# Optimization experiments

Hardware: AMD Instinct MI355X
Metric: run time of the kernel (lower is better)

The kernel has to match this reference:

```python
import jax, jax.numpy as jnp
import numpy as np

# Sizes (see shape_source): N samples, D=Config.dim, H=D//2, E question types, C classes/type
N, D, H, E, C = 65536, 768, 384, 8, 8


def setup_inputs() -> dict:
    key = jax.random.key(0)
    k_x, k_t, k_w1, k_w2 = jax.random.split(key, 4)
    x = jax.random.normal(k_x, (N, D), dtype=jnp.float32)
    question_types = jax.random.randint(k_t, (N,), 0, E, dtype=jnp.int32)
    # Stacked per-type MLP head parameters (E experts)
    W1 = jax.random.normal(k_w1, (E, D, H), dtype=jnp.float32) * 0.02
    b1 = jnp.zeros((E, H), dtype=jnp.float32)
    W2 = jax.random.normal(k_w2, (E, H, C), dtype=jnp.float32) * 0.02
    b2 = jnp.zeros((E, C), dtype=jnp.float32)
    return {"x": x, "W1": W1, "b1": b1, "W2": W2, "b2": b2,
            "question_types": question_types}


def reference(x, W1, b1, W2, b2, question_types):
    # Per-sample routed 2-layer MLP head: logits_i = MLP_{type_i}(x_i).
    # Dropout is eval-mode identity. Dense-per-expert compute + mask select
    # (standard MoE reference; E is a small fixed loop, not a data-dim loop).
    n_experts = W1.shape[0]
    out = jnp.zeros((x.shape[0], W2.shape[-1]), dtype=x.dtype)
    for e in range(n_experts):
        h = jax.nn.relu(x @ W1[e] + b1[e])        # [N, H]
        logits = h @ W2[e] + b2[e]                # [N, C]
        out = jnp.where((question_types == e)[:, None], logits, out)
    return out
```

## Files before the change

### kernel.cpp

```cpp
#include <hip/hip_runtime.h>

typedef short s16x8 __attribute__((ext_vector_type(8)));
typedef float f32x4 __attribute__((ext_vector_type(4)));

#define N_SAMPLES 65536
#define DIM 768
#define HID 384
#define NEXP 8
#define NCLS 8

#define WS_CNT    0
#define WS_BUCKET 1024
#define WS_W1T    (WS_BUCKET + NEXP * N_SAMPLES * 4)
#define WS_W2T    (WS_W1T + NEXP * HID * DIM * 2)

__device__ __forceinline__ unsigned short f2bf(float f) {
  union { float f; unsigned u; } v; v.f = f;
  unsigned r = v.u + 0x7fffu + ((v.u >> 16) & 1u);
  return (unsigned short)(r >> 16);
}

__global__ void k_transpose_w1(const float* __restrict__ W1,
                               unsigned short* __restrict__ W1T) {
  __shared__ float tile[32][33];
  const int e = blockIdx.z, k0 = blockIdx.x * 32, j0 = blockIdx.y * 32;
  const int tx = threadIdx.x, ty = threadIdx.y;
  const float* src = W1 + (size_t)e * DIM * HID;
#pragma unroll
  for (int i = 0; i < 32; i += 8)
    tile[ty + i][tx] = src[(size_t)(k0 + ty + i) * HID + j0 + tx];
  __syncthreads();
  unsigned short* dst = W1T + (size_t)e * HID * DIM;
#pragma unroll
  for (int i = 0; i < 32; i += 8)
    dst[(size_t)(j0 + ty + i) * DIM + k0 + tx] = f2bf(tile[tx][ty + i]);
}

__global__ void k_w2_cnt(const float* __restrict__ W2,
                         unsigned short* __restrict__ W2T,
                         int* __restrict__ cnt) {
  const int e = blockIdx.x, j = threadIdx.x;
  if (e == 0 && j < NEXP) cnt[j] = 0;
#pragma unroll
  for (int c = 0; c < NCLS; ++c)
    W2T[((size_t)e * NCLS + c) * HID + j] = f2bf(W2[((size_t)e * HID + j) * NCLS + c]);
}

__global__ void k_scatter_init(const int* __restrict__ qt, const float* __restrict__ b2,
                               int* __restrict__ cnt, int* __restrict__ bucket,
                               float* __restrict__ out) {
  __shared__ int lcnt[NEXP], lbase[NEXP];
  const int t = threadIdx.x;
  const int i = blockIdx.x * 256 + t;
  if (t < NEXP) lcnt[t] = 0;
  __syncthreads();
  const int e = qt[i];
  const int rank = atomicAdd(&lcnt[e], 1);
  __syncthreads();
  if (t < NEXP) lbase[t] = atomicAdd(&cnt[t], lcnt[t]);
  __syncthreads();
  bucket[(size_t)e * N_SAMPLES + lbase[e] + rank] = i;
  const float4* b2v = (const float4*)(b2 + e * NCLS);
  float4* ov = (float4*)(out + (size_t)i * NCLS);
  ov[0] = b2v[0];
  ov[1] = b2v[1];
}

#define GLL16(g, l)                                                        \
  __builtin_amdgcn_global_load_lds(                                        \
      (__attribute__((address_space(1))) void*)(void*)(g),                 \
      (__attribute__((address_space(3))) void*)(l), 16, 0, 0)

__global__ __launch_bounds__(256, 2) void k_moe_gemm(
    const float* __restrict__ x, const unsigned short* __restrict__ W1T,
    const float* __restrict__ b1, const unsigned short* __restrict__ W2T,
    const int* __restrict__ cnt, const int* __restrict__ bucket,
    float* __restrict__ out) {
  __shared__ __align__(16) short smem[17408];
  __shared__ __align__(16) short W2s[16 * 128];
  __shared__ float b1s[128];
  __shared__ int idxs[128];
  short* As = smem;
  short* Bs = smem + 4096;
  short* Hs = smem;

  const int e = blockIdx.z;
  const int n_e = cnt[e];
  const int j0 = blockIdx.x * 128;
  const int t = threadIdx.x;
  const int lane = t & 63;
  const int wave = t >> 6;
  const int lrow = lane & 15;
  const int quad = lane >> 4;
  const int lk = quad * 8;
  const int mbase = (wave & 1) * 64;
  const int nbase = (wave >> 1) * 64;

  {
    const int c = t >> 4, jj = (t & 15) * 8;
    s16x8 wv = {0, 0, 0, 0, 0, 0, 0, 0};
    if (c < NCLS) wv = *(const s16x8*)&W2T[((size_t)e * NCLS + c) * HID + j0 + jj];
    *(s16x8*)&W2s[c * 128 + jj] = wv;
  }
  if (t < 128) b1s[t] = b1[e * HID + j0 + t];

  for (int rt = blockIdx.y; rt * 128 < n_e; rt += gridDim.y) {
    const int row0 = rt * 128;
    __syncthreads();
    if (t < 128) {
      const int slot = row0 + t;
      idxs[t] = bucket[(size_t)e * N_SAMPLES + ((slot < n_e) ? slot : row0)];
    }
    __syncthreads();

    const float* xrow = x + (size_t)idxs[t >> 1] * DIM + (t & 1) * 16;
    const unsigned short* g0 = W1T + ((size_t)(e * HID + j0 + (t >> 2)) * DIM + (t & 3) * 8);
    const unsigned short* g1 = W1T + ((size_t)(e * HID + j0 + 64 + (t >> 2)) * DIM + (t & 3) * 8);

    f32x4 acc[4][4];
#pragma unroll
    for (int mi = 0; mi < 4; ++mi)
#pragma unroll
      for (int ni = 0; ni < 4; ++ni) acc[mi][ni] = (f32x4){0.f, 0.f, 0.f, 0.f};

    float4 v0 = ((const float4*)xrow)[0];
    float4 v1 = ((const float4*)xrow)[1];
    float4 v2 = ((const float4*)xrow)[2];
    float4 v3 = ((const float4*)xrow)[3];

    for (int ks = 0; ks < 24; ++ks) {
      s16x8 p0 = {(short)f2bf(v0.x), (short)f2bf(v0.y), (short)f2bf(v0.z), (short)f2bf(v0.w),
                  (short)f2bf(v1.x), (short)f2bf(v1.y), (short)f2bf(v1.z), (short)f2bf(v1.w)};
      s16x8 p1 = {(short)f2bf(v2.x), (short)f2bf(v2.y), (short)f2bf(v2.z), (short)f2bf(v2.w),
                  (short)f2bf(v3.x), (short)f2bf(v3.y), (short)f2bf(v3.z), (short)f2bf(v3.w)};
      *(s16x8*)&As[t * 16] = p0;
      *(s16x8*)&As[t * 16 + 8] = p1;
      GLL16(g0 + ks * 32, &Bs[t * 8]);
      GLL16(g1 + ks * 32, &Bs[2048 + t * 8]);
      __syncthreads();
      if (ks < 23) {
        const float4* nx = (const float4*)(xrow + (ks + 1) * 32);
        v0 = nx[0]; v1 = nx[1]; v2 = nx[2]; v3 = nx[3];
      }
      s16x8 bfr[4];
#pragma unroll
      for (int ni = 0; ni < 4; ++ni)
        bfr[ni] = *(const s16x8*)&Bs[(nbase + ni * 16 + lrow) * 32 + lk];
#pragma unroll
      for (int mi = 0; mi < 4; ++mi) {
        s16x8 afr = *(const s16x8*)&As[(mbase + mi * 16 + lrow) * 32 + lk];
#pragma unroll
        for (int ni = 0; ni < 4; ++ni)
          acc[mi][ni] = __builtin_amdgcn_mfma_f32_16x16x32_bf16(afr, bfr[ni], acc[mi][ni], 0, 0, 0);
      }
      __syncthreads();
    }

#pragma unroll
    for (int ni = 0; ni < 4; ++ni) {
      const int jl = nbase + ni * 16 + lrow;
      const float bias = b1s[jl];
#pragma unroll
      for (int mi = 0; mi < 4; ++mi) {
        const int mrow = mbase + mi * 16 + quad * 4;
#pragma unroll
        for (int r = 0; r < 4; ++r) {
          float v = acc[mi][ni][r] + bias;
          v = v > 0.f ? v : 0.f;
          Hs[(mrow + r) * 136 + jl] = (short)f2bf(v);
        }
      }
    }
    __syncthreads();

#pragma unroll
    for (int p = 0; p < 2; ++p) {
      const int mt = wave * 2 + p;
      f32x4 acc2 = (f32x4){0.f, 0.f, 0.f, 0.f};
#pragma unroll
      for (int kk = 0; kk < 4; ++kk) {
        s16x8 af = *(const s16x8*)&Hs[(mt * 16 + lrow) * 136 + kk * 32 + lk];
        s16x8 bf = *(const s16x8*)&W2s[lrow * 128 + kk * 32 + lk];
        acc2 = __builtin_amdgcn_mfma_f32_16x16x32_bf16(af, bf, acc2, 0, 0, 0);
      }
      if (lrow < NCLS) {
#pragma unroll
        for (int r = 0; r < 4; ++r) {
          const int m = mt * 16 + quad * 4 + r;
          if (row0 + m < n_e)
            atomicAdd(out + (size_t)idxs[m] * NCLS + lrow, acc2[r]);
        }
      }
    }
  }
}

extern "C" void kernel_launch(void* const* d_in, const int* in_sizes, int n_in,
                              void* d_out, int out_size, void* d_ws, size_t ws_size,
                              hipStream_t stream) {
  const float* x  = (const float*)d_in[0];
  const float* W1 = (const float*)d_in[1];
  const float* b1 = (const float*)d_in[2];
  const float* W2 = (const float*)d_in[3];
  const float* b2 = (const float*)d_in[4];
  const int* qt   = (const int*)d_in[5];
  float* out = (float*)d_out;
  char* ws = (char*)d_ws;

  int* cnt = (int*)(ws + WS_CNT);
  int* bucket = (int*)(ws + WS_BUCKET);
  unsigned short* W1T = (unsigned short*)(ws + WS_W1T);
  unsigned short* W2T = (unsigned short*)(ws + WS_W2T);

  k_transpose_w1<<<dim3(24, 12, 8), dim3(32, 8), 0, stream>>>(W1, W1T);
  k_w2_cnt<<<dim3(8), dim3(384), 0, stream>>>(W2, W2T, cnt);
  k_scatter_init<<<dim3(256), dim3(256), 0, stream>>>(qt, b2, cnt, bucket, out);
  k_moe_gemm<<<dim3(3, 96, 8), dim3(256), 0, stream>>>(x, W1T, b1, W2T, cnt, bucket, out);
}
```

Measured before the change: 377.9 us.

## Double-buffer GEMM LDS tiles, merge setup kernels, retune grid and occupancy

The main GEMM loop now keeps two LDS buffers for the A and B tiles. Each step issues the next W1 tile's global-to-LDS load and x prefetch, then runs the MFMAs on the current buffer, which leaves one barrier per k-step instead of two. The W2 transpose and counter zeroing move into the existing scatter and W1-transpose kernels, removing one launch. Launch bounds go from 2 to 3 blocks per CU and grid.y drops from 96 to 32, so each block loops over more row tiles. The tradeoffs are more LDS-resident state and higher register pressure at the raised occupancy target.

```diff
diff --git a/kernel.cpp b/kernel.cpp
--- a/kernel.cpp
+++ b/kernel.cpp
@@ -21,7 +21,11 @@
 }
 
 __global__ void k_transpose_w1(const float* __restrict__ W1,
-                               unsigned short* __restrict__ W1T) {
+                               unsigned short* __restrict__ W1T,
+                               int* __restrict__ cnt) {
+  if (blockIdx.x == 0 && blockIdx.y == 0 && blockIdx.z == 0 &&
+      threadIdx.y == 0 && threadIdx.x < NEXP)
+    cnt[threadIdx.x] = 0;
   __shared__ float tile[32][33];
   const int e = blockIdx.z, k0 = blockIdx.x * 32, j0 = blockIdx.y * 32;
   const int tx = threadIdx.x, ty = threadIdx.y;
@@ -36,21 +40,21 @@
     dst[(size_t)(j0 + ty + i) * DIM + k0 + tx] = f2bf(tile[tx][ty + i]);
 }
 
-__global__ void k_w2_cnt(const float* __restrict__ W2,
-                         unsigned short* __restrict__ W2T,
-                         int* __restrict__ cnt) {
-  const int e = blockIdx.x, j = threadIdx.x;
-  if (e == 0 && j < NEXP) cnt[j] = 0;
-#pragma unroll
-  for (int c = 0; c < NCLS; ++c)
-    W2T[((size_t)e * NCLS + c) * HID + j] = f2bf(W2[((size_t)e * HID + j) * NCLS + c]);
-}
-
 __global__ void k_scatter_init(const int* __restrict__ qt, const float* __restrict__ b2,
+                               const float* __restrict__ W2,
                                int* __restrict__ cnt, int* __restrict__ bucket,
-                               float* __restrict__ out) {
+                               float* __restrict__ out, unsigned short* __restrict__ W2T) {
+  const int t = threadIdx.x;
+  if (blockIdx.x >= 256) {
+    const int e = blockIdx.x - 256;
+    for (int j = t; j < HID; j += 256)
+#pragma unroll
+      for (int c = 0; c < NCLS; ++c)
+        W2T[((size_t)e * NCLS + c) * HID + j] =
+            f2bf(W2[((size_t)e * HID + j) * NCLS + c]);
+    return;
+  }
   __shared__ int lcnt[NEXP], lbase[NEXP];
-  const int t = threadIdx.x;
   const int i = blockIdx.x * 256 + t;
   if (t < NEXP) lcnt[t] = 0;
   __syncthreads();
@@ -71,7 +75,38 @@
       (__attribute__((address_space(1))) void*)(void*)(g),                 \
       (__attribute__((address_space(3))) void*)(l), 16, 0, 0)
 
-__global__ __launch_bounds__(256, 2) void k_moe_gemm(
+#define K_STEP(KS, AC, BC, BN)                                                  \
+  {                                                                             \
+    s16x8 p0 = {(short)f2bf(v0.x), (short)f2bf(v0.y), (short)f2bf(v0.z),        \
+                (short)f2bf(v0.w), (short)f2bf(v1.x), (short)f2bf(v1.y),        \
+                (short)f2bf(v1.z), (short)f2bf(v1.w)};                          \
+    s16x8 p1 = {(short)f2bf(v2.x), (short)f2bf(v2.y), (short)f2bf(v2.z),        \
+                (short)f2bf(v2.w), (short)f2bf(v3.x), (short)f2bf(v3.y),        \
+                (short)f2bf(v3.z), (short)f2bf(v3.w)};                          \
+    *(s16x8*)&(AC)[t * 16] = p0;                                                \
+    *(s16x8*)&(AC)[t * 16 + 8] = p1;                                            \
+    __syncthreads();                                                            \
+    if ((KS) + 1 < 24) {                                                        \
+      GLL16(g0 + ((KS) + 1) * 32, &(BN)[t * 8]);                                \
+      GLL16(g1 + ((KS) + 1) * 32, &(BN)[2048 + t * 8]);                         \
+      const float4* nx = (const float4*)(xrow + ((KS) + 1) * 32);               \
+      v0 = nx[0]; v1 = nx[1]; v2 = nx[2]; v3 = nx[3];                           \
+    }                                                                           \
+    s16x8 bfr[4];                                                               \
+    _Pragma("unroll")                                                           \
+    for (int ni = 0; ni < 4; ++ni)                                              \
+      bfr[ni] = *(const s16x8*)&(BC)[(nbase + ni * 16 + lrow) * 32 + lk];       \
+    _Pragma("unroll")                                                           \
+    for (int mi = 0; mi < 4; ++mi) {                                            \
+      s16x8 afr = *(const s16x8*)&(AC)[(mbase + mi * 16 + lrow) * 32 + lk];     \
+      _Pragma("unroll")                                                         \
+      for (int ni = 0; ni < 4; ++ni)                                            \
+        acc[mi][ni] = __builtin_amdgcn_mfma_f32_16x16x32_bf16(                  \
+            afr, bfr[ni], acc[mi][ni], 0, 0, 0);                                \
+    }                                                                           \
+  }
+
+__global__ __launch_bounds__(256, 3) void k_moe_gemm(
     const float* __restrict__ x, const unsigned short* __restrict__ W1T,
     const float* __restrict__ b1, const unsigned short* __restrict__ W2T,
     const int* __restrict__ cnt, const int* __restrict__ bucket,
@@ -80,8 +115,10 @@
   __shared__ __align__(16) short W2s[16 * 128];
   __shared__ float b1s[128];
   __shared__ int idxs[128];
-  short* As = smem;
-  short* Bs = smem + 4096;
+  short* As0 = smem;
+  short* As1 = smem + 4096;
+  short* Bs0 = smem + 8192;
+  short* Bs1 = smem + 12288;
   short* Hs = smem;
 
   const int e = blockIdx.z;
@@ -127,34 +164,15 @@
     float4 v1 = ((const float4*)xrow)[1];
     float4 v2 = ((const float4*)xrow)[2];
     float4 v3 = ((const float4*)xrow)[3];
-
-    for (int ks = 0; ks < 24; ++ks) {
-      s16x8 p0 = {(short)f2bf(v0.x), (short)f2bf(v0.y), (short)f2bf(v0.z), (short)f2bf(v0.w),
-                  (short)f2bf(v1.x), (short)f2bf(v1.y), (short)f2bf(v1.z), (short)f2bf(v1.w)};
-      s16x8 p1 = {(short)f2bf(v2.x), (short)f2bf(v2.y), (short)f2bf(v2.z), (short)f2bf(v2.w),
-                  (short)f2bf(v3.x), (short)f2bf(v3.y), (short)f2bf(v3.z), (short)f2bf(v3.w)};
-      *(s16x8*)&As[t * 16] = p0;
-      *(s16x8*)&As[t * 16 + 8] = p1;
-      GLL16(g0 + ks * 32, &Bs[t * 8]);
-      GLL16(g1 + ks * 32, &Bs[2048 + t * 8]);
-      __syncthreads();
-      if (ks < 23) {
-        const float4* nx = (const float4*)(xrow + (ks + 1) * 32);
-        v0 = nx[0]; v1 = nx[1]; v2 = nx[2]; v3 = nx[3];
-      }
-      s16x8 bfr[4];
-#pragma unroll
-      for (int ni = 0; ni < 4; ++ni)
-        bfr[ni] = *(const s16x8*)&Bs[(nbase + ni * 16 + lrow) * 32 + lk];
-#pragma unroll
-      for (int mi = 0; mi < 4; ++mi) {
-        s16x8 afr = *(const s16x8*)&As[(mbase + mi * 16 + lrow) * 32 + lk];
-#pragma unroll
-        for (int ni = 0; ni < 4; ++ni)
-          acc[mi][ni] = __builtin_amdgcn_mfma_f32_16x16x32_bf16(afr, bfr[ni], acc[mi][ni], 0, 0, 0);
-      }
-      __syncthreads();
-    }
+    GLL16(g0, &Bs0[t * 8]);
+    GLL16(g1, &Bs0[2048 + t * 8]);
+
+    for (int ks = 0; ks < 24; ks += 2) {
+      K_STEP(ks, As0, Bs0, Bs1)
+      K_STEP(ks + 1, As1, Bs1, Bs0)
+    }
+
+    __syncthreads();
 
 #pragma unroll
     for (int ni = 0; ni < 4; ++ni) {
@@ -212,8 +230,7 @@
   unsigned short* W1T = (unsigned short*)(ws + WS_W1T);
   unsigned short* W2T = (unsigned short*)(ws + WS_W2T);
 
-  k_transpose_w1<<<dim3(24, 12, 8), dim3(32, 8), 0, stream>>>(W1, W1T);
-  k_w2_cnt<<<dim3(8), dim3(384), 0, stream>>>(W2, W2T, cnt);
-  k_scatter_init<<<dim3(256), dim3(256), 0, stream>>>(qt, b2, cnt, bucket, out);
-  k_moe_gemm<<<dim3(3, 96, 8), dim3(256), 0, stream>>>(x, W1T, b1, W2T, cnt, bucket, out);
-}
+  k_transpose_w1<<<dim3(24, 12, 8), dim3(32, 8), 0, stream>>>(W1, W1T, cnt);
+  k_scatter_init<<<dim3(264), dim3(256), 0, stream>>>(qt, b2, W2, cnt, bucket, out, W2T);
+  k_moe_gemm<<<dim3(3, 32, 8), dim3(256), 0, stream>>>(x, W1T, b1, W2T, cnt, bucket, out);
+}
```

After: 382.7 us. About the same (+1.3%).

## Compute full hidden width per block to avoid x reloads and atomics

Applied to the files above, without the earlier changes.

Each block now covers all 384 hidden units for a 64-row tile of one expert, not a 128-column slice. Each x row is therefore read and converted to bf16 once instead of three times, and the second layer writes logits directly with the b2 bias instead of using atomicAdd onto a bias-initialised output. It adds LDS double buffering for the A and B tiles, a faster round-to-nearest bf16 packing via perm, and folds the W2 conversion and counter reset into other kernels, removing one launch. Per-block LDS use grows, and the bf16 rounding of activations changes slightly.

```diff
diff --git a/kernel.cpp b/kernel.cpp
--- a/kernel.cpp
+++ b/kernel.cpp
@@ -12,7 +12,6 @@
 #define WS_CNT    0
 #define WS_BUCKET 1024
 #define WS_W1T    (WS_BUCKET + NEXP * N_SAMPLES * 4)
-#define WS_W2T    (WS_W1T + NEXP * HID * DIM * 2)
 
 __device__ __forceinline__ unsigned short f2bf(float f) {
   union { float f; unsigned u; } v; v.f = f;
@@ -20,8 +19,23 @@
   return (unsigned short)(r >> 16);
 }
 
+__device__ __forceinline__ short f2bf_fast(float f) {
+  union { float f; unsigned u; } v; v.f = f;
+  return (short)((v.u + 0x8000u) >> 16);
+}
+
+__device__ __forceinline__ unsigned cvt2(float a, float b) {
+  union { float f; unsigned u; } ua, ub;
+  ua.f = a; ub.f = b;
+  return __builtin_amdgcn_perm(ub.u + 0x8000u, ua.u + 0x8000u, 0x07060302u);
+}
+
 __global__ void k_transpose_w1(const float* __restrict__ W1,
-                               unsigned short* __restrict__ W1T) {
+                               unsigned short* __restrict__ W1T,
+                               int* __restrict__ cnt) {
+  if (blockIdx.x == 0 && blockIdx.y == 0 && blockIdx.z == 0 &&
+      threadIdx.y == 0 && threadIdx.x < NEXP)
+    cnt[threadIdx.x] = 0;
   __shared__ float tile[32][33];
   const int e = blockIdx.z, k0 = blockIdx.x * 32, j0 = blockIdx.y * 32;
   const int tx = threadIdx.x, ty = threadIdx.y;
@@ -36,19 +50,8 @@
     dst[(size_t)(j0 + ty + i) * DIM + k0 + tx] = f2bf(tile[tx][ty + i]);
 }
 
-__global__ void k_w2_cnt(const float* __restrict__ W2,
-                         unsigned short* __restrict__ W2T,
-                         int* __restrict__ cnt) {
-  const int e = blockIdx.x, j = threadIdx.x;
-  if (e == 0 && j < NEXP) cnt[j] = 0;
-#pragma unroll
-  for (int c = 0; c < NCLS; ++c)
-    W2T[((size_t)e * NCLS + c) * HID + j] = f2bf(W2[((size_t)e * HID + j) * NCLS + c]);
-}
-
-__global__ void k_scatter_init(const int* __restrict__ qt, const float* __restrict__ b2,
-                               int* __restrict__ cnt, int* __restrict__ bucket,
-                               float* __restrict__ out) {
+__global__ void k_scatter(const int* __restrict__ qt, int* __restrict__ cnt,
+                          int* __restrict__ bucket) {
   __shared__ int lcnt[NEXP], lbase[NEXP];
   const int t = threadIdx.x;
   const int i = blockIdx.x * 256 + t;
@@ -60,10 +63,6 @@
   if (t < NEXP) lbase[t] = atomicAdd(&cnt[t], lcnt[t]);
   __syncthreads();
   bucket[(size_t)e * N_SAMPLES + lbase[e] + rank] = i;
-  const float4* b2v = (const float4*)(b2 + e * NCLS);
-  float4* ov = (float4*)(out + (size_t)i * NCLS);
-  ov[0] = b2v[0];
-  ov[1] = b2v[1];
 }
 
 #define GLL16(g, l)                                                        \
@@ -71,127 +70,143 @@
       (__attribute__((address_space(1))) void*)(void*)(g),                 \
       (__attribute__((address_space(3))) void*)(l), 16, 0, 0)
 
+#define GLLB(KS, BUF)                                                      \
+  _Pragma("unroll") for (int rep = 0; rep < 6; ++rep)                      \
+      GLL16(bp + (size_t)rep * 64 * DIM + (KS) * 32, &(BUF)[(rep * 256 + t) * 8]);
+
+#define ASTORE(BUF, LO, HI)                                                \
+  {                                                                        \
+    unsigned p01 = cvt2((LO).x, (LO).y), p23 = cvt2((LO).z, (LO).w);       \
+    unsigned p45 = cvt2((HI).x, (HI).y), p67 = cvt2((HI).z, (HI).w);       \
+    uint4 pk = {p01, p23, p45, p67};                                       \
+    *(uint4*)&(BUF)[ar * 40 + aq * 8] = pk;                                \
+  }
+
+#define COMPUTE(AS, BS)                                                    \
+  {                                                                        \
+    s16x8 bfr[6];                                                          \
+    _Pragma("unroll") for (int ni = 0; ni < 6; ++ni)                       \
+        bfr[ni] = *(const s16x8*)&(BS)[(wave * 96 + ni * 16 + lrow) * 32 + quad * 8]; \
+    _Pragma("unroll") for (int mi = 0; mi < 4; ++mi) {                     \
+      s16x8 afr = *(const s16x8*)&(AS)[(mi * 16 + lrow) * 40 + quad * 8];  \
+      _Pragma("unroll") for (int ni = 0; ni < 6; ++ni)                     \
+          acc[mi][ni] = __builtin_amdgcn_mfma_f32_16x16x32_bf16(           \
+              afr, bfr[ni], acc[mi][ni], 0, 0, 0);                         \
+    }                                                                      \
+  }
+
 __global__ __launch_bounds__(256, 2) void k_moe_gemm(
     const float* __restrict__ x, const unsigned short* __restrict__ W1T,
-    const float* __restrict__ b1, const unsigned short* __restrict__ W2T,
-    const int* __restrict__ cnt, const int* __restrict__ bucket,
-    float* __restrict__ out) {
-  __shared__ __align__(16) short smem[17408];
-  __shared__ __align__(16) short W2s[16 * 128];
-  __shared__ float b1s[128];
-  __shared__ int idxs[128];
-  short* As = smem;
-  short* Bs = smem + 4096;
-  short* Hs = smem;
-
-  const int e = blockIdx.z;
+    const float* __restrict__ b1, const float* __restrict__ W2,
+    const float* __restrict__ b2, const int* __restrict__ cnt,
+    const int* __restrict__ bucket, float* __restrict__ out) {
+  __shared__ __align__(16) short smem[29696];
+  __shared__ __align__(16) short W2s[16 * 392];
+  __shared__ float b1s[HID];
+  __shared__ float b2s[NCLS];
+  short* As0 = smem;
+  short* As1 = smem + 2560;
+  short* Bs0 = smem + 5120;
+  short* Bs1 = smem + 17408;
+  short* Hs  = smem;
+
+  const int e = blockIdx.x;
   const int n_e = cnt[e];
-  const int j0 = blockIdx.x * 128;
   const int t = threadIdx.x;
   const int lane = t & 63;
   const int wave = t >> 6;
   const int lrow = lane & 15;
   const int quad = lane >> 4;
-  const int lk = quad * 8;
-  const int mbase = (wave & 1) * 64;
-  const int nbase = (wave >> 1) * 64;
-
-  {
-    const int c = t >> 4, jj = (t & 15) * 8;
-    s16x8 wv = {0, 0, 0, 0, 0, 0, 0, 0};
-    if (c < NCLS) wv = *(const s16x8*)&W2T[((size_t)e * NCLS + c) * HID + j0 + jj];
-    *(s16x8*)&W2s[c * 128 + jj] = wv;
-  }
-  if (t < 128) b1s[t] = b1[e * HID + j0 + t];
-
-  for (int rt = blockIdx.y; rt * 128 < n_e; rt += gridDim.y) {
-    const int row0 = rt * 128;
+  const int ar = t >> 2;
+  const int aq = t & 3;
+
+  for (int j = t; j < HID; j += 256) {
+    b1s[j] = b1[e * HID + j];
+    const float* wr = W2 + ((size_t)e * HID + j) * NCLS;
+#pragma unroll
+    for (int c = 0; c < NCLS; ++c) W2s[c * 392 + j] = (short)f2bf(wr[c]);
+#pragma unroll
+    for (int c = NCLS; c < 16; ++c) W2s[c * 392 + j] = 0;
+  }
+  if (t < NCLS) b2s[t] = b2[e * NCLS + t];
+
+  const unsigned short* bp = W1T + ((size_t)e * HID + (t >> 2)) * DIM + (t & 3) * 8;
+
+  for (int rt = blockIdx.y; rt * 64 < n_e; rt += gridDim.y) {
+    const int row0 = rt * 64;
+    int slot = row0 + ar;
+    if (slot >= n_e) slot = n_e - 1;
+    const int aidx = bucket[(size_t)e * N_SAMPLES + slot];
+    const float* ap = x + (size_t)aidx * DIM + aq * 8;
+
+    f32x4 acc[4][6];
+#pragma unroll
+    for (int mi = 0; mi < 4; ++mi)
+#pragma unroll
+      for (int ni = 0; ni < 6; ++ni) acc[mi][ni] = (f32x4){0.f, 0.f, 0.f, 0.f};
+
+    float4 a0lo = ((const float4*)ap)[0];
+    float4 a0hi = ((const float4*)(ap + 4))[0];
+    GLLB(0, Bs0)
+    ASTORE(As0, a0lo, a0hi)
+    float4 a1lo = ((const float4*)(ap + 32))[0];
+    float4 a1hi = ((const float4*)(ap + 36))[0];
+
+    for (int ks = 0; ks < 24; ks += 2) {
+      __syncthreads();
+      if (ks + 1 < 24) { GLLB(ks + 1, Bs1) ASTORE(As1, a1lo, a1hi) }
+      if (ks + 2 < 24) {
+        a0lo = ((const float4*)(ap + (ks + 2) * 32))[0];
+        a0hi = ((const float4*)(ap + (ks + 2) * 32 + 4))[0];
+      }
+      COMPUTE(As0, Bs0)
+      __syncthreads();
+      if (ks + 2 < 24) { GLLB(ks + 2, Bs0) ASTORE(As0, a0lo, a0hi) }
+      if (ks + 3 < 24) {
+        a1lo = ((const float4*)(ap + (ks + 3) * 32))[0];
+        a1hi = ((const float4*)(ap + (ks + 3) * 32 + 4))[0];
+      }
+      COMPUTE(As1, Bs1)
+    }
+
     __syncthreads();
-    if (t < 128) {
-      const int slot = row0 + t;
-      idxs[t] = bucket[(size_t)e * N_SAMPLES + ((slot < n_e) ? slot : row0)];
-    }
-    __syncthreads();
-
-    const float* xrow = x + (size_t)idxs[t >> 1] * DIM + (t & 1) * 16;
-    const unsigned short* g0 = W1T + ((size_t)(e * HID + j0 + (t >> 2)) * DIM + (t & 3) * 8);
-    const unsigned short* g1 = W1T + ((size_t)(e * HID + j0 + 64 + (t >> 2)) * DIM + (t & 3) * 8);
-
-    f32x4 acc[4][4];
+
 #pragma unroll
     for (int mi = 0; mi < 4; ++mi)
 #pragma unroll
-      for (int ni = 0; ni < 4; ++ni) acc[mi][ni] = (f32x4){0.f, 0.f, 0.f, 0.f};
-
-    float4 v0 = ((const float4*)xrow)[0];
-    float4 v1 = ((const float4*)xrow)[1];
-    float4 v2 = ((const float4*)xrow)[2];
-    float4 v3 = ((const float4*)xrow)[3];
-
-    for (int ks = 0; ks < 24; ++ks) {
-      s16x8 p0 = {(short)f2bf(v0.x), (short)f2bf(v0.y), (short)f2bf(v0.z), (short)f2bf(v0.w),
-                  (short)f2bf(v1.x), (short)f2bf(v1.y), (short)f2bf(v1.z), (short)f2bf(v1.w)};
-      s16x8 p1 = {(short)f2bf(v2.x), (short)f2bf(v2.y), (short)f2bf(v2.z), (short)f2bf(v2.w),
-                  (short)f2bf(v3.x), (short)f2bf(v3.y), (short)f2bf(v3.z), (short)f2bf(v3.w)};
-      *(s16x8*)&As[t * 16] = p0;
-      *(s16x8*)&As[t * 16 + 8] = p1;
-      GLL16(g0 + ks * 32, &Bs[t * 8]);
-      GLL16(g1 + ks * 32, &Bs[2048 + t * 8]);
-      __syncthreads();
-      if (ks < 23) {
-        const float4* nx = (const float4*)(xrow + (ks + 1) * 32);
-        v0 = nx[0]; v1 = nx[1]; v2 = nx[2]; v3 = nx[3];
-      }
-      s16x8 bfr[4];
-#pragma unroll
-      for (int ni = 0; ni < 4; ++ni)
-        bfr[ni] = *(const s16x8*)&Bs[(nbase + ni * 16 + lrow) * 32 + lk];
-#pragma unroll
-      for (int mi = 0; mi < 4; ++mi) {
-        s16x8 afr = *(const s16x8*)&As[(mbase + mi * 16 + lrow) * 32 + lk];
-#pragma unroll
-        for (int ni = 0; ni < 4; ++ni)
-          acc[mi][ni] = __builtin_amdgcn_mfma_f32_16x16x32_bf16(afr, bfr[ni], acc[mi][ni], 0, 0, 0);
-      }
-      __syncthreads();
-    }
-
-#pragma unroll
-    for (int ni = 0; ni < 4; ++ni) {
-      const int jl = nbase + ni * 16 + lrow;
-      const float bias = b1s[jl];
-#pragma unroll
-      for (int mi = 0; mi < 4; ++mi) {
-        const int mrow = mbase + mi * 16 + quad * 4;
+      for (int ni = 0; ni < 6; ++ni) {
+        const int j = wave * 96 + ni * 16 + lrow;
+        const float bias = b1s[j];
 #pragma unroll
         for (int r = 0; r < 4; ++r) {
           float v = acc[mi][ni][r] + bias;
           v = v > 0.f ? v : 0.f;
-          Hs[(mrow + r) * 136 + jl] = (short)f2bf(v);
+          Hs[(mi * 16 + quad * 4 + r) * 392 + j] = f2bf_fast(v);
+        }
+      }
+    __syncthreads();
+
+    {
+      f32x4 acc2 = (f32x4){0.f, 0.f, 0.f, 0.f};
+#pragma unroll
+      for (int kk = 0; kk < 12; ++kk) {
+        s16x8 af = *(const s16x8*)&Hs[(wave * 16 + lrow) * 392 + kk * 32 + quad * 8];
+        s16x8 bf = *(const s16x8*)&W2s[lrow * 392 + kk * 32 + quad * 8];
+        acc2 = __builtin_amdgcn_mfma_f32_16x16x32_bf16(af, bf, acc2, 0, 0, 0);
+      }
+      if (lrow < NCLS) {
+        const float bb = b2s[lrow];
+#pragma unroll
+        for (int r = 0; r < 4; ++r) {
+          const int m = wave * 16 + quad * 4 + r;
+          if (row0 + m < n_e) {
+            const int oi = bucket[(size_t)e * N_SAMPLES + row0 + m];
+            out[(size_t)oi * NCLS + lrow] = acc2[r] + bb;
+          }
         }
       }
     }
     __syncthreads();
-
-#pragma unroll
-    for (int p = 0; p < 2; ++p) {
-      const int mt = wave * 2 + p;
-      f32x4 acc2 = (f32x4){0.f, 0.f, 0.f, 0.f};
-#pragma unroll
-      for (int kk = 0; kk < 4; ++kk) {
-        s16x8 af = *(const s16x8*)&Hs[(mt * 16 + lrow) * 136 + kk * 32 + lk];
-        s16x8 bf = *(const s16x8*)&W2s[lrow * 128 + kk * 32 + lk];
-        acc2 = __builtin_amdgcn_mfma_f32_16x16x32_bf16(af, bf, acc2, 0, 0, 0);
-      }
-      if (lrow < NCLS) {
-#pragma unroll
-        for (int r = 0; r < 4; ++r) {
-          const int m = mt * 16 + quad * 4 + r;
-          if (row0 + m < n_e)
-            atomicAdd(out + (size_t)idxs[m] * NCLS + lrow, acc2[r]);
-        }
-      }
-    }
   }
 }
 
@@ -210,10 +225,8 @@
   int* cnt = (int*)(ws + WS_CNT);
   int* bucket = (int*)(ws + WS_BUCKET);
   unsigned short* W1T = (unsigned short*)(ws + WS_W1T);
-  unsigned short* W2T = (unsigned short*)(ws + WS_W2T);
-
-  k_transpose_w1<<<dim3(24, 12, 8), dim3(32, 8), 0, stream>>>(W1, W1T);
-  k_w2_cnt<<<dim3(8), dim3(384), 0, stream>>>(W2, W2T, cnt);
-  k_scatter_init<<<dim3(256), dim3(256), 0, stream>>>(qt, b2, cnt, bucket, out);
-  k_moe_gemm<<<dim3(3, 96, 8), dim3(256), 0, stream>>>(x, W1T, b1, W2T, cnt, bucket, out);
-}
+
+  k_transpose_w1<<<dim3(24, 12, 8), dim3(32, 8), 0, stream>>>(W1, W1T, cnt);
+  k_scatter<<<dim3(256), dim3(256), 0, stream>>>(qt, cnt, bucket);
+  k_moe_gemm<<<dim3(8, 64), dim3(256), 0, stream>>>(x, W1T, b1, W2, b2, cnt, bucket, out);
+}
```

Measured after the change: 349.1 us. 1.08x faster.
